# Optimization experiments

Hardware: AMD Instinct MI355X
Metric: run time of the kernel (lower is better)

## Reference

```python
import jax, jax.numpy as jnp
import numpy as np

B, S, I, H = 256, 512, 128, 256
THR = 0.001  # silence_threshold


def _glorot(k, shape):
    # xavier_uniform over the last two dims (matches nn.init.xavier_uniform_)
    fan_out, fan_in = shape[-2], shape[-1]
    lim = float(np.sqrt(6.0 / (fan_in + fan_out)))
    return jax.random.uniform(k, shape, jnp.float32, -lim, lim)


def setup_inputs() -> dict:
    key = jax.random.key(0)
    ks = jax.random.split(key, 8)
    # gate order along leading axis 0: [f, i, o, c]
    b_enc = jnp.concatenate([jnp.ones((1, H), jnp.float32), jnp.zeros((3, H), jnp.float32)], axis=0)
    return {
        "x": jax.random.normal(ks[0], (B, S, I), jnp.float32),
        # encoder: input->hidden and hidden->hidden weights (+ Linear biases + extra b_* params)
        "enc_Wx": _glorot(ks[1], (4, H, I)),
        "enc_bx": jnp.zeros((4, H), jnp.float32),
        "enc_Wh": _glorot(ks[2], (4, H, H)),
        "enc_bh": jnp.zeros((4, H), jnp.float32),
        "enc_b": b_enc,
        # decoder: its input_size == hidden_size
        "dec_Wx": _glorot(ks[3], (4, H, H)),
        "dec_bx": jnp.zeros((4, H), jnp.float32),
        "dec_Wh": _glorot(ks[4], (4, H, H)),
        "dec_bh": jnp.zeros((4, H), jnp.float32),
        "dec_b": b_enc,
        # reconstruct Linear(hidden_size -> input_size)
        "rec_W": _glorot(ks[5], (I, H)),
        "rec_b": jnp.zeros((I,), jnp.float32),
    }


def _cell(x, h, c, Wx, bx, Wh, bh, b):
    # fused gate GEMMs: g[k] = x @ Wx[k].T + bx[k] + h @ Wh[k].T + bh[k] + b[k]
    g = (jnp.einsum('bi,ghi->gbh', x, Wx) + bx[:, None, :]
         + jnp.einsum('bh,gkh->gbk', h, Wh) + bh[:, None, :]
         + b[:, None, :])  # [4, B, H]
    f_t = jax.nn.sigmoid(g[0])
    i_t = jax.nn.sigmoid(g[1])
    o_t = jax.nn.sigmoid(g[2])
    c_tilde = jnp.tanh(g[3])
    # silence mask on L2 norm over feature dim
    active = (jnp.linalg.norm(x, axis=1, keepdims=True) > THR).astype(x.dtype)
    c_next = f_t * c + i_t * c + active * (i_t * c_tilde)
    h_next = o_t * jnp.tanh(c_next)
    return h_next, c_next


def reference(x, enc_Wx, enc_bx, enc_Wh, enc_bh, enc_b,
              dec_Wx, dec_bx, dec_Wh, dec_bh, dec_b, rec_W, rec_b):
    Bsz, Slen = x.shape[0], x.shape[1]
    h0 = jnp.zeros((Bsz, H), x.dtype)
    c0 = jnp.zeros((Bsz, H), x.dtype)

    def enc_step(carry, xt):
        h, c = carry
        h, c = _cell(xt, h, c, enc_Wx, enc_bx, enc_Wh, enc_bh, enc_b)
        return (h, c), None

    (h_enc, c_enc), _ = jax.lax.scan(enc_step, (h0, c0), jnp.swapaxes(x, 0, 1))

    # in the decoder, decoder_input always equals h_prev (h fed back as input)
    def dec_step(carry, _):
        h, c = carry
        h, c = _cell(h, h, c, dec_Wx, dec_bx, dec_Wh, dec_bh, dec_b)
        out = h @ rec_W.T + rec_b  # [B, I]
        return (h, c), out

    _, outs = jax.lax.scan(dec_step, (h_enc, c_enc), None, length=Slen)
    return jnp.swapaxes(outs, 0, 1)  # [B, S, I]
```

## Files before the change

### kernel.cpp

```cpp
#include <hip/hip_runtime.h>
#include <cmath>

#define kB 256
#define kS 512
#define kI 128
#define kH 256

typedef __attribute__((ext_vector_type(8))) short short8;
typedef __attribute__((ext_vector_type(4))) float f32x4;
typedef unsigned long long u64;

#define AS_STRIDE 408

#define WS_HX_U64 (2 * 16 * 16 * 256)

__device__ __forceinline__ float sigmoidf_(float z) { return 1.0f / (1.0f + expf(-z)); }

__device__ __forceinline__ unsigned short f2b(float f) {
  unsigned u = __builtin_bit_cast(unsigned, f);
  unsigned r = (u + 0x7fffu + ((u >> 16) & 1u)) >> 16;
  return (unsigned short)r;
}
__device__ __forceinline__ float b2f(unsigned short s) {
  unsigned u = ((unsigned)s) << 16;
  return __builtin_bit_cast(float, u);
}
__device__ __forceinline__ void bsplit2(float f, unsigned short& h_, unsigned short& l_) {
  h_ = f2b(f);
  l_ = f2b(f - b2f(h_));
}
__device__ __forceinline__ void bsplit3(float f, unsigned short& h_, unsigned short& m_, unsigned short& l_) {
  h_ = f2b(f);
  float r1 = f - b2f(h_);
  m_ = f2b(r1);
  l_ = f2b(r1 - b2f(m_));
}

__device__ __forceinline__ void pollrow8(const u64* grp, int col, int rbase,
                                         unsigned seq16, u64* u) {
  unsigned miss = 0xffu;
  for (;;) {
    unsigned nm = 0;
#pragma unroll
    for (int j = 0; j < 8; ++j)
      if (miss & (1u << j))
        u[j] = __hip_atomic_load(grp + (size_t)(rbase + j) * 256 + col,
                                 __ATOMIC_RELAXED, __HIP_MEMORY_SCOPE_SYSTEM);
#pragma unroll
    for (int j = 0; j < 8; ++j)
      if ((miss & (1u << j)) && (unsigned)(u[j] >> 48) != seq16) nm |= 1u << j;
    if (!nm) return;
    miss = nm;
    __builtin_amdgcn_s_sleep(1);
  }
}

__launch_bounds__(512, 2)
__global__ void lstm_mfma(const float* __restrict__ x,
                          const float* __restrict__ enc_Wx, const float* __restrict__ enc_bx,
                          const float* __restrict__ enc_Wh, const float* __restrict__ enc_bh,
                          const float* __restrict__ enc_b,
                          const float* __restrict__ dec_Wx, const float* __restrict__ dec_bx,
                          const float* __restrict__ dec_Wh, const float* __restrict__ dec_bh,
                          const float* __restrict__ dec_b,
                          const float* __restrict__ rec_W, const float* __restrict__ rec_b,
                          float* __restrict__ out,
                          u64* __restrict__ hx) {
  __shared__ __align__(16) short As_h[16 * AS_STRIDE];
  __shared__ __align__(16) short As_m[16 * AS_STRIDE];
  __shared__ __align__(16) short As_l[16 * AS_STRIDE];
  __shared__ float g_scr[8 * 16 * 17];
  __shared__ float r_scr[8 * 16 * 17];
  __shared__ float red[16][16];
  __shared__ float maskS[16];

  const int tid = threadIdx.x;
  const int bt = blockIdx.x & 15;
  const int ht = blockIdx.x >> 4;
  const int b0 = bt << 4, hh0 = ht << 5;
  const int w  = tid >> 6;
  const int l  = tid & 63;
  const int fr = l & 15;
  const int gq = l >> 4;
  const int cb = tid >> 5;
  const int cq = tid & 31;
  const int hhc = hh0 + cq;
  const int col  = tid & 255;
  const int rbase = (tid >> 8) * 8;

  float be0 = enc_bx[0*kH+hhc] + enc_bh[0*kH+hhc] + enc_b[0*kH+hhc];
  float be1 = enc_bx[1*kH+hhc] + enc_bh[1*kH+hhc] + enc_b[1*kH+hhc];
  float be2 = enc_bx[2*kH+hhc] + enc_bh[2*kH+hhc] + enc_b[2*kH+hhc];
  float be3 = enc_bx[3*kH+hhc] + enc_bh[3*kH+hhc] + enc_b[3*kH+hhc];
  float bd0 = dec_bx[0*kH+hhc] + dec_bh[0*kH+hhc] + dec_b[0*kH+hhc];
  float bd1 = dec_bx[1*kH+hhc] + dec_bh[1*kH+hhc] + dec_b[1*kH+hhc];
  float bd2 = dec_bx[2*kH+hhc] + dec_bh[2*kH+hhc] + dec_b[2*kH+hhc];
  float bd3 = dec_bx[3*kH+hhc] + dec_bh[3*kH+hhc] + dec_b[3*kH+hhc];
  float recb = (ht < 4) ? rec_b[ht * 32 + cq] : 0.0f;
  float creg = 0.0f;

  const int g  = w & 3;
  const int hw = hh0 + ((w >> 2) << 4) + fr;
  short8 wfh[12], wfm[12], wfl[12];
#pragma unroll
  for (int kst = 0; kst < 12; ++kst) {
    int k = kst * 32 + gq * 8;
    const float* src = (k < 128)
        ? (enc_Wx + ((size_t)(g * kH) + hw) * kI + k)
        : (enc_Wh + ((size_t)(g * kH) + hw) * kH + (k - 128));
    short8 hi, mi, lo;
#pragma unroll
    for (int j = 0; j < 8; ++j) {
      unsigned short h_, m_, l_;
      bsplit3(src[j], h_, m_, l_);
      hi[j] = (short)h_; mi[j] = (short)m_; lo[j] = (short)l_;
    }
    wfh[kst] = hi; wfm[kst] = mi; wfl[kst] = lo;
  }

  for (int s = 0; s < kS; ++s) {
    const int par = s & 1;
    if (tid < 256 && (tid & 15) < 8) {
      const int xb = tid >> 4, xq = tid & 15;
      const float* xp = x + ((size_t)(b0 + xb) * kS + s) * kI + xq * 16;
      float arr[16];
      *(float4*)(arr + 0)  = *(const float4*)(xp + 0);
      *(float4*)(arr + 4)  = *(const float4*)(xp + 4);
      *(float4*)(arr + 8)  = *(const float4*)(xp + 8);
      *(float4*)(arr + 12) = *(const float4*)(xp + 12);
      float ss = 0.f;
      short8 H0, H1, M0, M1, L0, L1;
#pragma unroll
      for (int j = 0; j < 16; ++j) {
        float v = arr[j];
        ss += v * v;
        unsigned short h_, m_, l_;
        bsplit3(v, h_, m_, l_);
        if (j < 8) { H0[j] = (short)h_; M0[j] = (short)m_; L0[j] = (short)l_; }
        else       { H1[j-8] = (short)h_; M1[j-8] = (short)m_; L1[j-8] = (short)l_; }
      }
      *(short8*)(As_h + xb * AS_STRIDE + xq * 16)     = H0;
      *(short8*)(As_h + xb * AS_STRIDE + xq * 16 + 8) = H1;
      *(short8*)(As_m + xb * AS_STRIDE + xq * 16)     = M0;
      *(short8*)(As_m + xb * AS_STRIDE + xq * 16 + 8) = M1;
      *(short8*)(As_l + xb * AS_STRIDE + xq * 16)     = L0;
      *(short8*)(As_l + xb * AS_STRIDE + xq * 16 + 8) = L1;
      red[xb][xq] = ss;
    }
    {
      const u64* grp = hx + ((size_t)(par * 16 + bt) * 16) * 256;
      u64 u[8];
      pollrow8(grp, col, rbase, (unsigned)(s & 0xffff), u);
#pragma unroll
      for (int j = 0; j < 8; ++j) {
        As_h[(rbase + j) * AS_STRIDE + 128 + col] = (short)(unsigned short)(u[j] >> 32);
        As_m[(rbase + j) * AS_STRIDE + 128 + col] = (short)(unsigned short)(u[j] >> 16);
        As_l[(rbase + j) * AS_STRIDE + 128 + col] = (short)(unsigned short)(u[j]);
      }
    }
    __syncthreads();
    if (tid < 16) {
      float ss = 0.f;
#pragma unroll
      for (int j = 0; j < 8; ++j) ss += red[tid][j];
      maskS[tid] = (ss > 1e-6f) ? 1.0f : 0.0f;
    }
    f32x4 a0 = {0.f,0.f,0.f,0.f}, a1 = a0, a2 = a0, a3 = a0, a4 = a0, a5 = a0;
#pragma unroll
    for (int kst = 0; kst < 12; ++kst) {
      const short8 ah = *(const short8*)(As_h + fr * AS_STRIDE + kst * 32 + gq * 8);
      const short8 am = *(const short8*)(As_m + fr * AS_STRIDE + kst * 32 + gq * 8);
      const short8 al = *(const short8*)(As_l + fr * AS_STRIDE + kst * 32 + gq * 8);
      a0 = __builtin_amdgcn_mfma_f32_16x16x32_bf16(ah, wfh[kst], a0, 0, 0, 0);
      a1 = __builtin_amdgcn_mfma_f32_16x16x32_bf16(ah, wfm[kst], a1, 0, 0, 0);
      a2 = __builtin_amdgcn_mfma_f32_16x16x32_bf16(am, wfh[kst], a2, 0, 0, 0);
      a3 = __builtin_amdgcn_mfma_f32_16x16x32_bf16(ah, wfl[kst], a3, 0, 0, 0);
      a4 = __builtin_amdgcn_mfma_f32_16x16x32_bf16(am, wfm[kst], a4, 0, 0, 0);
      a5 = __builtin_amdgcn_mfma_f32_16x16x32_bf16(al, wfh[kst], a5, 0, 0, 0);
    }
    f32x4 d = (((a5 + a4) + a3) + (a2 + a1)) + a0;
#pragma unroll
    for (int i = 0; i < 4; ++i) g_scr[(w * 16 + gq * 4 + i) * 17 + fr] = d[i];
    __syncthreads();
    {
      const int hsub = (cq >> 4) * 4, fq = cq & 15;
      float gf = g_scr[((0 + hsub) * 16 + cb) * 17 + fq] + be0;
      float gi = g_scr[((1 + hsub) * 16 + cb) * 17 + fq] + be1;
      float go = g_scr[((2 + hsub) * 16 + cb) * 17 + fq] + be2;
      float gc = g_scr[((3 + hsub) * 16 + cb) * 17 + fq] + be3;
      float m  = maskS[cb];
      float f_ = sigmoidf_(gf), i_ = sigmoidf_(gi), o_ = sigmoidf_(go);
      float ct = tanhf(gc);
      creg = (f_ + i_) * creg + m * (i_ * ct);
      float hval = o_ * tanhf(creg);
      unsigned short hb, mb2, lb;
      bsplit3(hval, hb, mb2, lb);
      u64 pk = ((u64)(unsigned)((s + 1) & 0xffff) << 48) | ((u64)hb << 32) | ((u64)mb2 << 16) | (u64)lb;
      size_t wi = (((size_t)(((s + 1) & 1) * 16 + bt) * 16 + cb) * 256) + hhc;
      __hip_atomic_store(hx + wi, pk, __ATOMIC_RELAXED, __HIP_MEMORY_SCOPE_SYSTEM);
    }
  }

  short8 dwh[8], dwm[8], dwl[8];
#pragma unroll
  for (int kst = 0; kst < 8; ++kst) {
    int k = kst * 32 + gq * 8;
    const float* s1 = dec_Wx + ((size_t)(g * kH) + hw) * kH + k;
    const float* s2 = dec_Wh + ((size_t)(g * kH) + hw) * kH + k;
    short8 hi, mi, lo;
#pragma unroll
    for (int j = 0; j < 8; ++j) {
      unsigned short h_, m_, l_;
      bsplit3(s1[j] + s2[j], h_, m_, l_);
      hi[j] = (short)h_; mi[j] = (short)m_; lo[j] = (short)l_;
    }
    dwh[kst] = hi; dwm[kst] = mi; dwl[kst] = lo;
  }
  short8 rfh[2], rfl[2];
#pragma unroll
  for (int kk = 0; kk < 2; ++kk) {
    short8 hi = {0,0,0,0,0,0,0,0}, lo = hi;
    if (ht < 4) {
      int k = (2 * (w & 3) + kk) * 32 + gq * 8;
      const float* src = rec_W + ((size_t)(ht * 32 + ((w >> 2) << 4) + fr)) * kH + k;
#pragma unroll
      for (int j = 0; j < 8; ++j) {
        unsigned short h_, l_;
        bsplit2(src[j], h_, l_);
        hi[j] = (short)h_; lo[j] = (short)l_;
      }
    }
    rfh[kk] = hi; rfl[kk] = lo;
  }

  for (int t = 0; t < kS; ++t) {
    const int s = kS + t;
    const int par = s & 1;
    {
      const u64* grp = hx + ((size_t)(par * 16 + bt) * 16) * 256;
      u64 u[8];
      pollrow8(grp, col, rbase, (unsigned)(s & 0xffff), u);
#pragma unroll
      for (int j = 0; j < 8; ++j) {
        As_h[(rbase + j) * AS_STRIDE + col] = (short)(unsigned short)(u[j] >> 32);
        As_m[(rbase + j) * AS_STRIDE + col] = (short)(unsigned short)(u[j] >> 16);
        As_l[(rbase + j) * AS_STRIDE + col] = (short)(unsigned short)(u[j]);
      }
    }
    __syncthreads();
    if (tid < 256) {
      const int mb = tid >> 4, mq = tid & 15;
      float ss = 0.f;
#pragma unroll
      for (int g2 = 0; g2 < 2; ++g2) {
        const short8 hv = *(const short8*)(As_h + mb * AS_STRIDE + mq * 16 + g2 * 8);
        const short8 mv = *(const short8*)(As_m + mb * AS_STRIDE + mq * 16 + g2 * 8);
        const short8 lv = *(const short8*)(As_l + mb * AS_STRIDE + mq * 16 + g2 * 8);
#pragma unroll
        for (int j = 0; j < 8; ++j) {
          float v = b2f((unsigned short)hv[j]) + b2f((unsigned short)mv[j]) + b2f((unsigned short)lv[j]);
          ss += v * v;
        }
      }
      red[mb][mq] = ss;
    }
    __syncthreads();
    if (tid < 16) {
      float ss = 0.f;
#pragma unroll
      for (int j = 0; j < 16; ++j) ss += red[tid][j];
      maskS[tid] = (ss > 1e-6f) ? 1.0f : 0.0f;
    }
    f32x4 a0 = {0.f,0.f,0.f,0.f}, a1 = a0, a2 = a0, a3 = a0, a4 = a0, a5 = a0;
#pragma unroll
    for (int kst = 0; kst < 8; ++kst) {
      const short8 ah = *(const short8*)(As_h + fr * AS_STRIDE + kst * 32 + gq * 8);
      const short8 am = *(const short8*)(As_m + fr * AS_STRIDE + kst * 32 + gq * 8);
      const short8 al = *(const short8*)(As_l + fr * AS_STRIDE + kst * 32 + gq * 8);
      a0 = __builtin_amdgcn_mfma_f32_16x16x32_bf16(ah, dwh[kst], a0, 0, 0, 0);
      a1 = __builtin_amdgcn_mfma_f32_16x16x32_bf16(ah, dwm[kst], a1, 0, 0, 0);
      a2 = __builtin_amdgcn_mfma_f32_16x16x32_bf16(am, dwh[kst], a2, 0, 0, 0);
      a3 = __builtin_amdgcn_mfma_f32_16x16x32_bf16(ah, dwl[kst], a3, 0, 0, 0);
      a4 = __builtin_amdgcn_mfma_f32_16x16x32_bf16(am, dwm[kst], a4, 0, 0, 0);
      a5 = __builtin_amdgcn_mfma_f32_16x16x32_bf16(al, dwh[kst], a5, 0, 0, 0);
    }
    f32x4 d = (((a5 + a4) + a3) + (a2 + a1)) + a0;
#pragma unroll
    for (int i = 0; i < 4; ++i) g_scr[(w * 16 + gq * 4 + i) * 17 + fr] = d[i];
    if (ht < 4) {
      f32x4 r0 = {0.f,0.f,0.f,0.f}, r1 = r0, r2 = r0;
#pragma unroll
      for (int kk = 0; kk < 2; ++kk) {
        const short8 ah = *(const short8*)(As_h + fr * AS_STRIDE + (2 * (w & 3) + kk) * 32 + gq * 8);
        const short8 am = *(const short8*)(As_m + fr * AS_STRIDE + (2 * (w & 3) + kk) * 32 + gq * 8);
        r0 = __builtin_amdgcn_mfma_f32_16x16x32_bf16(ah, rfh[kk], r0, 0, 0, 0);
        r1 = __builtin_amdgcn_mfma_f32_16x16x32_bf16(ah, rfl[kk], r1, 0, 0, 0);
        r2 = __builtin_amdgcn_mfma_f32_16x16x32_bf16(am, rfh[kk], r2, 0, 0, 0);
      }
      f32x4 rd = r0 + r1 + r2;
#pragma unroll
      for (int i = 0; i < 4; ++i) r_scr[(w * 16 + gq * 4 + i) * 17 + fr] = rd[i];
    }
    __syncthreads();
    {
      const int hsub = (cq >> 4) * 4, fq = cq & 15;
      float gf = g_scr[((0 + hsub) * 16 + cb) * 17 + fq] + bd0;
      float gi = g_scr[((1 + hsub) * 16 + cb) * 17 + fq] + bd1;
      float go = g_scr[((2 + hsub) * 16 + cb) * 17 + fq] + bd2;
      float gc = g_scr[((3 + hsub) * 16 + cb) * 17 + fq] + bd3;
      float m  = maskS[cb];
      float f_ = sigmoidf_(gf), i_ = sigmoidf_(gi), o_ = sigmoidf_(go);
      float ct = tanhf(gc);
      creg = (f_ + i_) * creg + m * (i_ * ct);
      float hval = o_ * tanhf(creg);
      unsigned short hb, mb2, lb;
      bsplit3(hval, hb, mb2, lb);
      u64 pk = ((u64)(unsigned)((s + 1) & 0xffff) << 48) | ((u64)hb << 32) | ((u64)mb2 << 16) | (u64)lb;
      size_t wi = (((size_t)(((s + 1) & 1) * 16 + bt) * 16 + cb) * 256) + hhc;
      __hip_atomic_store(hx + wi, pk, __ATOMIC_RELAXED, __HIP_MEMORY_SCOPE_SYSTEM);
    }
    if (ht < 4 && t > 0) {
      const int c2 = cq >> 4, fq = cq & 15;
      float rsum = r_scr[((c2 * 4 + 0) * 16 + cb) * 17 + fq]
                 + r_scr[((c2 * 4 + 1) * 16 + cb) * 17 + fq]
                 + r_scr[((c2 * 4 + 2) * 16 + cb) * 17 + fq]
                 + r_scr[((c2 * 4 + 3) * 16 + cb) * 17 + fq] + recb;
      __builtin_nontemporal_store(rsum, &out[((size_t)(b0 + cb) * kS + (t - 1)) * kI + ht * 32 + cq]);
    }
  }

  {
    {
      const u64* grp = hx + ((size_t)(0 * 16 + bt) * 16) * 256;
      u64 u[8];
      pollrow8(grp, col, rbase, (unsigned)((2 * kS) & 0xffff), u);
#pragma unroll
      for (int j = 0; j < 8; ++j) {
        As_h[(rbase + j) * AS_STRIDE + col] = (short)(unsigned short)(u[j] >> 32);
        As_m[(rbase + j) * AS_STRIDE + col] = (short)(unsigned short)(u[j] >> 16);
      }
    }
    __syncthreads();
    if (ht < 4) {
      f32x4 r0 = {0.f,0.f,0.f,0.f}, r1 = r0, r2 = r0;
#pragma unroll
      for (int kk = 0; kk < 2; ++kk) {
        const short8 ah = *(const short8*)(As_h + fr * AS_STRIDE + (2 * (w & 3) + kk) * 32 + gq * 8);
        const short8 am = *(const short8*)(As_m + fr * AS_STRIDE + (2 * (w & 3) + kk) * 32 + gq * 8);
        r0 = __builtin_amdgcn_mfma_f32_16x16x32_bf16(ah, rfh[kk], r0, 0, 0, 0);
        r1 = __builtin_amdgcn_mfma_f32_16x16x32_bf16(ah, rfl[kk], r1, 0, 0, 0);
        r2 = __builtin_amdgcn_mfma_f32_16x16x32_bf16(am, rfh[kk], r2, 0, 0, 0);
      }
      f32x4 rd = r0 + r1 + r2;
#pragma unroll
      for (int i = 0; i < 4; ++i) r_scr[(w * 16 + gq * 4 + i) * 17 + fr] = rd[i];
    }
    __syncthreads();
    if (ht < 4) {
      const int c2 = cq >> 4, fq = cq & 15;
      float rsum = r_scr[((c2 * 4 + 0) * 16 + cb) * 17 + fq]
                 + r_scr[((c2 * 4 + 1) * 16 + cb) * 17 + fq]
                 + r_scr[((c2 * 4 + 2) * 16 + cb) * 17 + fq]
                 + r_scr[((c2 * 4 + 3) * 16 + cb) * 17 + fq] + recb;
      __builtin_nontemporal_store(rsum, &out[((size_t)(b0 + cb) * kS + (kS - 1)) * kI + ht * 32 + cq]);
    }
  }
}

extern "C" void kernel_launch(void* const* d_in, const int* in_sizes, int n_in,
                              void* d_out, int out_size, void* d_ws, size_t ws_size,
                              hipStream_t stream) {
  const float* x      = (const float*)d_in[0];
  const float* enc_Wx = (const float*)d_in[1];
  const float* enc_bx = (const float*)d_in[2];
  const float* enc_Wh = (const float*)d_in[3];
  const float* enc_bh = (const float*)d_in[4];
  const float* enc_b  = (const float*)d_in[5];
  const float* dec_Wx = (const float*)d_in[6];
  const float* dec_bx = (const float*)d_in[7];
  const float* dec_Wh = (const float*)d_in[8];
  const float* dec_bh = (const float*)d_in[9];
  const float* dec_b  = (const float*)d_in[10];
  const float* rec_W  = (const float*)d_in[11];
  const float* rec_b  = (const float*)d_in[12];
  float* out = (float*)d_out;

  u64* hx = (u64*)d_ws;

  hipMemsetAsync(d_ws, 0, (size_t)WS_HX_U64 * 8, stream);

  hipLaunchKernelGGL(lstm_mfma, dim3(128), dim3(512), 0, stream,
                     x, enc_Wx, enc_bx, enc_Wh, enc_bh, enc_b,
                     dec_Wx, dec_bx, dec_Wh, dec_bh, dec_b,
                     rec_W, rec_b, out, hx);
}
```

Measured before the change: 3.755 ms.

## Split gate GEMM along K across waves with two h-subtiles per wave

Each wave now computes two 16-column h subtiles over half of the K dimension instead of one subtile over full K, so each LDS A-fragment load feeds twice as many MFMAs. Partial gate sums from the two K halves are reduced through an enlarged LDS scratch before the cell update. The x load/bf16 split is spread over all 512 threads with float4 loads, and the reconstruct projection is split along K across all 8 waves with an 8-way sum. This adds accumulator registers and extra LDS reads in the reduction.

```diff
diff --git a/kernel.cpp b/kernel.cpp
--- a/kernel.cpp
+++ b/kernel.cpp
@@ -7,10 +7,12 @@
 #define kH 256
 
 typedef __attribute__((ext_vector_type(8))) short short8;
+typedef __attribute__((ext_vector_type(4))) short short4v;
 typedef __attribute__((ext_vector_type(4))) float f32x4;
 typedef unsigned long long u64;
 
 #define AS_STRIDE 408
+#define GSTR 18
 
 #define WS_HX_U64 (2 * 16 * 16 * 256)
 
@@ -55,23 +57,24 @@
   }
 }
 
-__launch_bounds__(512, 2)
-__global__ void lstm_mfma(const float* __restrict__ x,
-                          const float* __restrict__ enc_Wx, const float* __restrict__ enc_bx,
-                          const float* __restrict__ enc_Wh, const float* __restrict__ enc_bh,
-                          const float* __restrict__ enc_b,
-                          const float* __restrict__ dec_Wx, const float* __restrict__ dec_bx,
-                          const float* __restrict__ dec_Wh, const float* __restrict__ dec_bh,
-                          const float* __restrict__ dec_b,
-                          const float* __restrict__ rec_W, const float* __restrict__ rec_b,
-                          float* __restrict__ out,
-                          u64* __restrict__ hx) {
+__global__ void __launch_bounds__(512)
+__attribute__((amdgpu_waves_per_eu(2, 2)))
+lstm_mfma(const float* __restrict__ x,
+          const float* __restrict__ enc_Wx, const float* __restrict__ enc_bx,
+          const float* __restrict__ enc_Wh, const float* __restrict__ enc_bh,
+          const float* __restrict__ enc_b,
+          const float* __restrict__ dec_Wx, const float* __restrict__ dec_bx,
+          const float* __restrict__ dec_Wh, const float* __restrict__ dec_bh,
+          const float* __restrict__ dec_b,
+          const float* __restrict__ rec_W, const float* __restrict__ rec_b,
+          float* __restrict__ out,
+          u64* __restrict__ hx) {
   __shared__ __align__(16) short As_h[16 * AS_STRIDE];
   __shared__ __align__(16) short As_m[16 * AS_STRIDE];
   __shared__ __align__(16) short As_l[16 * AS_STRIDE];
-  __shared__ float g_scr[8 * 16 * 17];
-  __shared__ float r_scr[8 * 16 * 17];
-  __shared__ float red[16][16];
+  __shared__ float g_scr[16 * 16 * GSTR];
+  __shared__ float r_scr[16 * 16 * GSTR];
+  __shared__ float red[16][32];
   __shared__ float maskS[16];
 
   const int tid = threadIdx.x;
@@ -79,6 +82,8 @@
   const int ht = blockIdx.x >> 4;
   const int b0 = bt << 4, hh0 = ht << 5;
   const int w  = tid >> 6;
+  const int g  = w & 3;
+  const int kh = w >> 2;
   const int l  = tid & 63;
   const int fr = l & 15;
   const int gq = l >> 4;
@@ -99,12 +104,13 @@
   float recb = (ht < 4) ? rec_b[ht * 32 + cq] : 0.0f;
   float creg = 0.0f;
 
-  const int g  = w & 3;
-  const int hw = hh0 + ((w >> 2) << 4) + fr;
-  short8 wfh[12], wfm[12], wfl[12];
-#pragma unroll
-  for (int kst = 0; kst < 12; ++kst) {
-    int k = kst * 32 + gq * 8;
+  short8 wfh[2][6], wfm[2][6], wfl[2][6];
+#pragma unroll
+  for (int st = 0; st < 2; ++st)
+#pragma unroll
+  for (int kl = 0; kl < 6; ++kl) {
+    int k = (kh * 6 + kl) * 32 + gq * 8;
+    const int hw = hh0 + st * 16 + fr;
     const float* src = (k < 128)
         ? (enc_Wx + ((size_t)(g * kH) + hw) * kI + k)
         : (enc_Wh + ((size_t)(g * kH) + hw) * kH + (k - 128));
@@ -115,37 +121,30 @@
       bsplit3(src[j], h_, m_, l_);
       hi[j] = (short)h_; mi[j] = (short)m_; lo[j] = (short)l_;
     }
-    wfh[kst] = hi; wfm[kst] = mi; wfl[kst] = lo;
+    wfh[st][kl] = hi; wfm[st][kl] = mi; wfl[st][kl] = lo;
   }
 
   for (int s = 0; s < kS; ++s) {
     const int par = s & 1;
-    if (tid < 256 && (tid & 15) < 8) {
-      const int xb = tid >> 4, xq = tid & 15;
-      const float* xp = x + ((size_t)(b0 + xb) * kS + s) * kI + xq * 16;
-      float arr[16];
-      *(float4*)(arr + 0)  = *(const float4*)(xp + 0);
-      *(float4*)(arr + 4)  = *(const float4*)(xp + 4);
-      *(float4*)(arr + 8)  = *(const float4*)(xp + 8);
-      *(float4*)(arr + 12) = *(const float4*)(xp + 12);
+    {
+      const int xb = tid >> 5, xc = (tid & 31) * 4;
+      const float* xp = x + ((size_t)(b0 + xb) * kS + s) * kI + xc;
+      float4 xv = *(const float4*)xp;
+      float arr[4] = {xv.x, xv.y, xv.z, xv.w};
+      short4v hv, mv, lv;
       float ss = 0.f;
-      short8 H0, H1, M0, M1, L0, L1;
-#pragma unroll
-      for (int j = 0; j < 16; ++j) {
+#pragma unroll
+      for (int j = 0; j < 4; ++j) {
         float v = arr[j];
         ss += v * v;
         unsigned short h_, m_, l_;
         bsplit3(v, h_, m_, l_);
-        if (j < 8) { H0[j] = (short)h_; M0[j] = (short)m_; L0[j] = (short)l_; }
-        else       { H1[j-8] = (short)h_; M1[j-8] = (short)m_; L1[j-8] = (short)l_; }
-      }
-      *(short8*)(As_h + xb * AS_STRIDE + xq * 16)     = H0;
-      *(short8*)(As_h + xb * AS_STRIDE + xq * 16 + 8) = H1;
-      *(short8*)(As_m + xb * AS_STRIDE + xq * 16)     = M0;
-      *(short8*)(As_m + xb * AS_STRIDE + xq * 16 + 8) = M1;
-      *(short8*)(As_l + xb * AS_STRIDE + xq * 16)     = L0;
-      *(short8*)(As_l + xb * AS_STRIDE + xq * 16 + 8) = L1;
-      red[xb][xq] = ss;
+        hv[j] = (short)h_; mv[j] = (short)m_; lv[j] = (short)l_;
+      }
+      *(short4v*)(As_h + xb * AS_STRIDE + xc) = hv;
+      *(short4v*)(As_m + xb * AS_STRIDE + xc) = mv;
+      *(short4v*)(As_l + xb * AS_STRIDE + xc) = lv;
+      red[xb][tid & 31] = ss;
     }
     {
       const u64* grp = hx + ((size_t)(par * 16 + bt) * 16) * 256;
@@ -162,32 +161,44 @@
     if (tid < 16) {
       float ss = 0.f;
 #pragma unroll
-      for (int j = 0; j < 8; ++j) ss += red[tid][j];
+      for (int j = 0; j < 32; ++j) ss += red[tid][j];
       maskS[tid] = (ss > 1e-6f) ? 1.0f : 0.0f;
     }
-    f32x4 a0 = {0.f,0.f,0.f,0.f}, a1 = a0, a2 = a0, a3 = a0, a4 = a0, a5 = a0;
-#pragma unroll
-    for (int kst = 0; kst < 12; ++kst) {
-      const short8 ah = *(const short8*)(As_h + fr * AS_STRIDE + kst * 32 + gq * 8);
-      const short8 am = *(const short8*)(As_m + fr * AS_STRIDE + kst * 32 + gq * 8);
-      const short8 al = *(const short8*)(As_l + fr * AS_STRIDE + kst * 32 + gq * 8);
-      a0 = __builtin_amdgcn_mfma_f32_16x16x32_bf16(ah, wfh[kst], a0, 0, 0, 0);
-      a1 = __builtin_amdgcn_mfma_f32_16x16x32_bf16(ah, wfm[kst], a1, 0, 0, 0);
-      a2 = __builtin_amdgcn_mfma_f32_16x16x32_bf16(am, wfh[kst], a2, 0, 0, 0);
-      a3 = __builtin_amdgcn_mfma_f32_16x16x32_bf16(ah, wfl[kst], a3, 0, 0, 0);
-      a4 = __builtin_amdgcn_mfma_f32_16x16x32_bf16(am, wfm[kst], a4, 0, 0, 0);
-      a5 = __builtin_amdgcn_mfma_f32_16x16x32_bf16(al, wfh[kst], a5, 0, 0, 0);
-    }
-    f32x4 d = (((a5 + a4) + a3) + (a2 + a1)) + a0;
-#pragma unroll
-    for (int i = 0; i < 4; ++i) g_scr[(w * 16 + gq * 4 + i) * 17 + fr] = d[i];
-    __syncthreads();
-    {
-      const int hsub = (cq >> 4) * 4, fq = cq & 15;
-      float gf = g_scr[((0 + hsub) * 16 + cb) * 17 + fq] + be0;
-      float gi = g_scr[((1 + hsub) * 16 + cb) * 17 + fq] + be1;
-      float go = g_scr[((2 + hsub) * 16 + cb) * 17 + fq] + be2;
-      float gc = g_scr[((3 + hsub) * 16 + cb) * 17 + fq] + be3;
+    f32x4 acc[2][6];
+#pragma unroll
+    for (int st = 0; st < 2; ++st)
+#pragma unroll
+    for (int i = 0; i < 6; ++i) acc[st][i] = (f32x4){0.f, 0.f, 0.f, 0.f};
+#pragma unroll
+    for (int kl = 0; kl < 6; ++kl) {
+      const int ko = (kh * 6 + kl) * 32 + gq * 8;
+      const short8 ah = *(const short8*)(As_h + fr * AS_STRIDE + ko);
+      const short8 am = *(const short8*)(As_m + fr * AS_STRIDE + ko);
+      const short8 al = *(const short8*)(As_l + fr * AS_STRIDE + ko);
+#pragma unroll
+      for (int st = 0; st < 2; ++st) {
+        acc[st][0] = __builtin_amdgcn_mfma_f32_16x16x32_bf16(ah, wfh[st][kl], acc[st][0], 0, 0, 0);
+        acc[st][1] = __builtin_amdgcn_mfma_f32_16x16x32_bf16(ah, wfm[st][kl], acc[st][1], 0, 0, 0);
+        acc[st][2] = __builtin_amdgcn_mfma_f32_16x16x32_bf16(am, wfh[st][kl], acc[st][2], 0, 0, 0);
+        acc[st][3] = __builtin_amdgcn_mfma_f32_16x16x32_bf16(ah, wfl[st][kl], acc[st][3], 0, 0, 0);
+        acc[st][4] = __builtin_amdgcn_mfma_f32_16x16x32_bf16(am, wfm[st][kl], acc[st][4], 0, 0, 0);
+        acc[st][5] = __builtin_amdgcn_mfma_f32_16x16x32_bf16(al, wfh[st][kl], acc[st][5], 0, 0, 0);
+      }
+    }
+#pragma unroll
+    for (int st = 0; st < 2; ++st) {
+      f32x4 d = (((acc[st][5] + acc[st][4]) + acc[st][3]) + (acc[st][2] + acc[st][1])) + acc[st][0];
+      const int ti = (kh * 4 + g) * 2 + st;
+#pragma unroll
+      for (int i = 0; i < 4; ++i) g_scr[(ti * 16 + gq * 4 + i) * GSTR + fr] = d[i];
+    }
+    __syncthreads();
+    {
+      const int st = cq >> 4, fq = cq & 15;
+      float gf = g_scr[(((0*4+0)*2+st)*16+cb)*GSTR+fq] + g_scr[(((1*4+0)*2+st)*16+cb)*GSTR+fq] + be0;
+      float gi = g_scr[(((0*4+1)*2+st)*16+cb)*GSTR+fq] + g_scr[(((1*4+1)*2+st)*16+cb)*GSTR+fq] + be1;
+      float go = g_scr[(((0*4+2)*2+st)*16+cb)*GSTR+fq] + g_scr[(((1*4+2)*2+st)*16+cb)*GSTR+fq] + be2;
+      float gc = g_scr[(((0*4+3)*2+st)*16+cb)*GSTR+fq] + g_scr[(((1*4+3)*2+st)*16+cb)*GSTR+fq] + be3;
       float m  = maskS[cb];
       float f_ = sigmoidf_(gf), i_ = sigmoidf_(gi), o_ = sigmoidf_(go);
       float ct = tanhf(gc);
@@ -201,10 +212,13 @@
     }
   }
 
-  short8 dwh[8], dwm[8], dwl[8];
-#pragma unroll
-  for (int kst = 0; kst < 8; ++kst) {
-    int k = kst * 32 + gq * 8;
+  short8 dwh[2][4], dwm[2][4], dwl[2][4];
+#pragma unroll
+  for (int st = 0; st < 2; ++st)
+#pragma unroll
+  for (int kl = 0; kl < 4; ++kl) {
+    int k = (kh * 4 + kl) * 32 + gq * 8;
+    const int hw = hh0 + st * 16 + fr;
     const float* s1 = dec_Wx + ((size_t)(g * kH) + hw) * kH + k;
     const float* s2 = dec_Wh + ((size_t)(g * kH) + hw) * kH + k;
     short8 hi, mi, lo;
@@ -214,15 +228,15 @@
       bsplit3(s1[j] + s2[j], h_, m_, l_);
       hi[j] = (short)h_; mi[j] = (short)m_; lo[j] = (short)l_;
     }
-    dwh[kst] = hi; dwm[kst] = mi; dwl[kst] = lo;
+    dwh[st][kl] = hi; dwm[st][kl] = mi; dwl[st][kl] = lo;
   }
   short8 rfh[2], rfl[2];
 #pragma unroll
-  for (int kk = 0; kk < 2; ++kk) {
+  for (int st = 0; st < 2; ++st) {
     short8 hi = {0,0,0,0,0,0,0,0}, lo = hi;
     if (ht < 4) {
-      int k = (2 * (w & 3) + kk) * 32 + gq * 8;
-      const float* src = rec_W + ((size_t)(ht * 32 + ((w >> 2) << 4) + fr)) * kH + k;
+      int k = w * 32 + gq * 8;
+      const float* src = rec_W + ((size_t)(ht * 32 + st * 16 + fr)) * kH + k;
 #pragma unroll
       for (int j = 0; j < 8; ++j) {
         unsigned short h_, l_;
@@ -230,7 +244,7 @@
         hi[j] = (short)h_; lo[j] = (short)l_;
       }
     }
-    rfh[kk] = hi; rfl[kk] = lo;
+    rfh[st] = hi; rfl[st] = lo;
   }
 
   for (int t = 0; t < kS; ++t) {
@@ -271,43 +285,56 @@
       for (int j = 0; j < 16; ++j) ss += red[tid][j];
       maskS[tid] = (ss > 1e-6f) ? 1.0f : 0.0f;
     }
-    f32x4 a0 = {0.f,0.f,0.f,0.f}, a1 = a0, a2 = a0, a3 = a0, a4 = a0, a5 = a0;
-#pragma unroll
-    for (int kst = 0; kst < 8; ++kst) {
-      const short8 ah = *(const short8*)(As_h + fr * AS_STRIDE + kst * 32 + gq * 8);
-      const short8 am = *(const short8*)(As_m + fr * AS_STRIDE + kst * 32 + gq * 8);
-      const short8 al = *(const short8*)(As_l + fr * AS_STRIDE + kst * 32 + gq * 8);
-      a0 = __builtin_amdgcn_mfma_f32_16x16x32_bf16(ah, dwh[kst], a0, 0, 0, 0);
-      a1 = __builtin_amdgcn_mfma_f32_16x16x32_bf16(ah, dwm[kst], a1, 0, 0, 0);
-      a2 = __builtin_amdgcn_mfma_f32_16x16x32_bf16(am, dwh[kst], a2, 0, 0, 0);
-      a3 = __builtin_amdgcn_mfma_f32_16x16x32_bf16(ah, dwl[kst], a3, 0, 0, 0);
-      a4 = __builtin_amdgcn_mfma_f32_16x16x32_bf16(am, dwm[kst], a4, 0, 0, 0);
-      a5 = __builtin_amdgcn_mfma_f32_16x16x32_bf16(al, dwh[kst], a5, 0, 0, 0);
-    }
-    f32x4 d = (((a5 + a4) + a3) + (a2 + a1)) + a0;
-#pragma unroll
-    for (int i = 0; i < 4; ++i) g_scr[(w * 16 + gq * 4 + i) * 17 + fr] = d[i];
+    f32x4 acc[2][6];
+#pragma unroll
+    for (int st = 0; st < 2; ++st)
+#pragma unroll
+    for (int i = 0; i < 6; ++i) acc[st][i] = (f32x4){0.f, 0.f, 0.f, 0.f};
+#pragma unroll
+    for (int kl = 0; kl < 4; ++kl) {
+      const int ko = (kh * 4 + kl) * 32 + gq * 8;
+      const short8 ah = *(const short8*)(As_h + fr * AS_STRIDE + ko);
+      const short8 am = *(const short8*)(As_m + fr * AS_STRIDE + ko);
+      const short8 al = *(const short8*)(As_l + fr * AS_STRIDE + ko);
+#pragma unroll
+      for (int st = 0; st < 2; ++st) {
+        acc[st][0] = __builtin_amdgcn_mfma_f32_16x16x32_bf16(ah, dwh[st][kl], acc[st][0], 0, 0, 0);
+        acc[st][1] = __builtin_amdgcn_mfma_f32_16x16x32_bf16(ah, dwm[st][kl], acc[st][1], 0, 0, 0);
+        acc[st][2] = __builtin_amdgcn_mfma_f32_16x16x32_bf16(am, dwh[st][kl], acc[st][2], 0, 0, 0);
+        acc[st][3] = __builtin_amdgcn_mfma_f32_16x16x32_bf16(ah, dwl[st][kl], acc[st][3], 0, 0, 0);
+        acc[st][4] = __builtin_amdgcn_mfma_f32_16x16x32_bf16(am, dwm[st][kl], acc[st][4], 0, 0, 0);
+        acc[st][5] = __builtin_amdgcn_mfma_f32_16x16x32_bf16(al, dwh[st][kl], acc[st][5], 0, 0, 0);
+      }
+    }
+#pragma unroll
+    for (int st = 0; st < 2; ++st) {
+      f32x4 d = (((acc[st][5] + acc[st][4]) + acc[st][3]) + (acc[st][2] + acc[st][1])) + acc[st][0];
+      const int ti = (kh * 4 + g) * 2 + st;
+#pragma unroll
+      for (int i = 0; i < 4; ++i) g_scr[(ti * 16 + gq * 4 + i) * GSTR + fr] = d[i];
+    }
     if (ht < 4) {
-      f32x4 r0 = {0.f,0.f,0.f,0.f}, r1 = r0, r2 = r0;
-#pragma unroll
-      for (int kk = 0; kk < 2; ++kk) {
-        const short8 ah = *(const short8*)(As_h + fr * AS_STRIDE + (2 * (w & 3) + kk) * 32 + gq * 8);
-        const short8 am = *(const short8*)(As_m + fr * AS_STRIDE + (2 * (w & 3) + kk) * 32 + gq * 8);
-        r0 = __builtin_amdgcn_mfma_f32_16x16x32_bf16(ah, rfh[kk], r0, 0, 0, 0);
-        r1 = __builtin_amdgcn_mfma_f32_16x16x32_bf16(ah, rfl[kk], r1, 0, 0, 0);
-        r2 = __builtin_amdgcn_mfma_f32_16x16x32_bf16(am, rfh[kk], r2, 0, 0, 0);
-      }
-      f32x4 rd = r0 + r1 + r2;
-#pragma unroll
-      for (int i = 0; i < 4; ++i) r_scr[(w * 16 + gq * 4 + i) * 17 + fr] = rd[i];
-    }
-    __syncthreads();
-    {
-      const int hsub = (cq >> 4) * 4, fq = cq & 15;
-      float gf = g_scr[((0 + hsub) * 16 + cb) * 17 + fq] + bd0;
-      float gi = g_scr[((1 + hsub) * 16 + cb) * 17 + fq] + bd1;
-      float go = g_scr[((2 + hsub) * 16 + cb) * 17 + fq] + bd2;
-      float gc = g_scr[((3 + hsub) * 16 + cb) * 17 + fq] + bd3;
+      const int ko = w * 32 + gq * 8;
+      const short8 ah = *(const short8*)(As_h + fr * AS_STRIDE + ko);
+      const short8 am = *(const short8*)(As_m + fr * AS_STRIDE + ko);
+#pragma unroll
+      for (int st = 0; st < 2; ++st) {
+        f32x4 r0 = {0.f,0.f,0.f,0.f}, r1 = r0, r2 = r0;
+        r0 = __builtin_amdgcn_mfma_f32_16x16x32_bf16(ah, rfh[st], r0, 0, 0, 0);
+        r1 = __builtin_amdgcn_mfma_f32_16x16x32_bf16(ah, rfl[st], r1, 0, 0, 0);
+        r2 = __builtin_amdgcn_mfma_f32_16x16x32_bf16(am, rfh[st], r2, 0, 0, 0);
+        f32x4 rd = r0 + r1 + r2;
+#pragma unroll
+        for (int i = 0; i < 4; ++i) r_scr[((w * 2 + st) * 16 + gq * 4 + i) * GSTR + fr] = rd[i];
+      }
+    }
+    __syncthreads();
+    {
+      const int st = cq >> 4, fq = cq & 15;
+      float gf = g_scr[(((0*4+0)*2+st)*16+cb)*GSTR+fq] + g_scr[(((1*4+0)*2+st)*16+cb)*GSTR+fq] + bd0;
+      float gi = g_scr[(((0*4+1)*2+st)*16+cb)*GSTR+fq] + g_scr[(((1*4+1)*2+st)*16+cb)*GSTR+fq] + bd1;
+      float go = g_scr[(((0*4+2)*2+st)*16+cb)*GSTR+fq] + g_scr[(((1*4+2)*2+st)*16+cb)*GSTR+fq] + bd2;
+      float gc = g_scr[(((0*4+3)*2+st)*16+cb)*GSTR+fq] + g_scr[(((1*4+3)*2+st)*16+cb)*GSTR+fq] + bd3;
       float m  = maskS[cb];
       float f_ = sigmoidf_(gf), i_ = sigmoidf_(gi), o_ = sigmoidf_(go);
       float ct = tanhf(gc);
@@ -320,11 +347,11 @@
       __hip_atomic_store(hx + wi, pk, __ATOMIC_RELAXED, __HIP_MEMORY_SCOPE_SYSTEM);
     }
     if (ht < 4 && t > 0) {
-      const int c2 = cq >> 4, fq = cq & 15;
-      float rsum = r_scr[((c2 * 4 + 0) * 16 + cb) * 17 + fq]
-                 + r_scr[((c2 * 4 + 1) * 16 + cb) * 17 + fq]
-                 + r_scr[((c2 * 4 + 2) * 16 + cb) * 17 + fq]
-                 + r_scr[((c2 * 4 + 3) * 16 + cb) * 17 + fq] + recb;
+      const int st = cq >> 4, fq = cq & 15;
+      float rsum = recb;
+#pragma unroll
+      for (int ww = 0; ww < 8; ++ww)
+        rsum += r_scr[((ww * 2 + st) * 16 + cb) * GSTR + fq];
       __builtin_nontemporal_store(rsum, &out[((size_t)(b0 + cb) * kS + (t - 1)) * kI + ht * 32 + cq]);
     }
   }
@@ -342,26 +369,27 @@
     }
     __syncthreads();
     if (ht < 4) {
-      f32x4 r0 = {0.f,0.f,0.f,0.f}, r1 = r0, r2 = r0;
-#pragma unroll
-      for (int kk = 0; kk < 2; ++kk) {
-        const short8 ah = *(const short8*)(As_h + fr * AS_STRIDE + (2 * (w & 3) + kk) * 32 + gq * 8);
-        const short8 am = *(const short8*)(As_m + fr * AS_STRIDE + (2 * (w & 3) + kk) * 32 + gq * 8);
-        r0 = __builtin_amdgcn_mfma_f32_16x16x32_bf16(ah, rfh[kk], r0, 0, 0, 0);
-        r1 = __builtin_amdgcn_mfma_f32_16x16x32_bf16(ah, rfl[kk], r1, 0, 0, 0);
-        r2 = __builtin_amdgcn_mfma_f32_16x16x32_bf16(am, rfh[kk], r2, 0, 0, 0);
-      }
-      f32x4 rd = r0 + r1 + r2;
-#pragma unroll
-      for (int i = 0; i < 4; ++i) r_scr[(w * 16 + gq * 4 + i) * 17 + fr] = rd[i];
+      const int ko = w * 32 + gq * 8;
+      const short8 ah = *(const short8*)(As_h + fr * AS_STRIDE + ko);
+      const short8 am = *(const short8*)(As_m + fr * AS_STRIDE + ko);
+#pragma unroll
+      for (int st = 0; st < 2; ++st) {
+        f32x4 r0 = {0.f,0.f,0.f,0.f}, r1 = r0, r2 = r0;
+        r0 = __builtin_amdgcn_mfma_f32_16x16x32_bf16(ah, rfh[st], r0, 0, 0, 0);
+        r1 = __builtin_amdgcn_mfma_f32_16x16x32_bf16(ah, rfl[st], r1, 0, 0, 0);
+        r2 = __builtin_amdgcn_mfma_f32_16x16x32_bf16(am, rfh[st], r2, 0, 0, 0);
+        f32x4 rd = r0 + r1 + r2;
+#pragma unroll
+        for (int i = 0; i < 4; ++i) r_scr[((w * 2 + st) * 16 + gq * 4 + i) * GSTR + fr] = rd[i];
+      }
     }
     __syncthreads();
     if (ht < 4) {
-      const int c2 = cq >> 4, fq = cq & 15;
-      float rsum = r_scr[((c2 * 4 + 0) * 16 + cb) * 17 + fq]
-                 + r_scr[((c2 * 4 + 1) * 16 + cb) * 17 + fq]
-                 + r_scr[((c2 * 4 + 2) * 16 + cb) * 17 + fq]
-                 + r_scr[((c2 * 4 + 3) * 16 + cb) * 17 + fq] + recb;
+      const int st = cq >> 4, fq = cq & 15;
+      float rsum = recb;
+#pragma unroll
+      for (int ww = 0; ww < 8; ++ww)
+        rsum += r_scr[((ww * 2 + st) * 16 + cb) * GSTR + fq];
       __builtin_nontemporal_store(rsum, &out[((size_t)(b0 + cb) * kS + (kS - 1)) * kI + ht * 32 + cq]);
     }
   }
```

New measurement: 4.746 ms. 26.4% more time.

## Overlap x-part MFMAs with hidden-state polling and spread x load over all threads

Applied to the files above, without the earlier changes.

In the encoder loop, all 512 threads now load and split x with one float4 each, not 128 threads with 16 each. A barrier then lets the x-input MFMAs (k-steps 0-3) run before the cross-block poll for the previous hidden state, so that part of the GEMM overlaps the wait. The decoder norm reduction is likewise spread over all threads with one short8 per array. This adds an extra barrier per encoder step and a wider reduction buffer.

```diff
diff --git a/kernel.cpp b/kernel.cpp
--- a/kernel.cpp
+++ b/kernel.cpp
@@ -7,6 +7,7 @@
 #define kH 256
 
 typedef __attribute__((ext_vector_type(8))) short short8;
+typedef __attribute__((ext_vector_type(4))) short short4v;
 typedef __attribute__((ext_vector_type(4))) float f32x4;
 typedef unsigned long long u64;
 
@@ -71,7 +72,7 @@
   __shared__ __align__(16) short As_l[16 * AS_STRIDE];
   __shared__ float g_scr[8 * 16 * 17];
   __shared__ float r_scr[8 * 16 * 17];
-  __shared__ float red[16][16];
+  __shared__ float red[16][32];
   __shared__ float maskS[16];
 
   const int tid = threadIdx.x;
@@ -120,32 +121,39 @@
 
   for (int s = 0; s < kS; ++s) {
     const int par = s & 1;
-    if (tid < 256 && (tid & 15) < 8) {
-      const int xb = tid >> 4, xq = tid & 15;
-      const float* xp = x + ((size_t)(b0 + xb) * kS + s) * kI + xq * 16;
-      float arr[16];
-      *(float4*)(arr + 0)  = *(const float4*)(xp + 0);
-      *(float4*)(arr + 4)  = *(const float4*)(xp + 4);
-      *(float4*)(arr + 8)  = *(const float4*)(xp + 8);
-      *(float4*)(arr + 12) = *(const float4*)(xp + 12);
+    {
+      const int xb = tid >> 5, xc = (tid & 31) * 4;
+      const float* xp = x + ((size_t)(b0 + xb) * kS + s) * kI + xc;
+      float4 xv = *(const float4*)xp;
+      float arr[4] = {xv.x, xv.y, xv.z, xv.w};
+      short4v hv, mv, lv;
       float ss = 0.f;
-      short8 H0, H1, M0, M1, L0, L1;
-#pragma unroll
-      for (int j = 0; j < 16; ++j) {
+#pragma unroll
+      for (int j = 0; j < 4; ++j) {
         float v = arr[j];
         ss += v * v;
         unsigned short h_, m_, l_;
         bsplit3(v, h_, m_, l_);
-        if (j < 8) { H0[j] = (short)h_; M0[j] = (short)m_; L0[j] = (short)l_; }
-        else       { H1[j-8] = (short)h_; M1[j-8] = (short)m_; L1[j-8] = (short)l_; }
-      }
-      *(short8*)(As_h + xb * AS_STRIDE + xq * 16)     = H0;
-      *(short8*)(As_h + xb * AS_STRIDE + xq * 16 + 8) = H1;
-      *(short8*)(As_m + xb * AS_STRIDE + xq * 16)     = M0;
-      *(short8*)(As_m + xb * AS_STRIDE + xq * 16 + 8) = M1;
-      *(short8*)(As_l + xb * AS_STRIDE + xq * 16)     = L0;
-      *(short8*)(As_l + xb * AS_STRIDE + xq * 16 + 8) = L1;
-      red[xb][xq] = ss;
+        hv[j] = (short)h_; mv[j] = (short)m_; lv[j] = (short)l_;
+      }
+      *(short4v*)(As_h + xb * AS_STRIDE + xc) = hv;
+      *(short4v*)(As_m + xb * AS_STRIDE + xc) = mv;
+      *(short4v*)(As_l + xb * AS_STRIDE + xc) = lv;
+      red[xb][tid & 31] = ss;
+    }
+    __syncthreads();
+    f32x4 a0 = {0.f,0.f,0.f,0.f}, a1 = a0, a2 = a0, a3 = a0, a4 = a0, a5 = a0;
+#pragma unroll
+    for (int kst = 0; kst < 4; ++kst) {
+      const short8 ah = *(const short8*)(As_h + fr * AS_STRIDE + kst * 32 + gq * 8);
+      const short8 am = *(const short8*)(As_m + fr * AS_STRIDE + kst * 32 + gq * 8);
+      const short8 al = *(const short8*)(As_l + fr * AS_STRIDE + kst * 32 + gq * 8);
+      a0 = __builtin_amdgcn_mfma_f32_16x16x32_bf16(ah, wfh[kst], a0, 0, 0, 0);
+      a1 = __builtin_amdgcn_mfma_f32_16x16x32_bf16(ah, wfm[kst], a1, 0, 0, 0);
+      a2 = __builtin_amdgcn_mfma_f32_16x16x32_bf16(am, wfh[kst], a2, 0, 0, 0);
+      a3 = __builtin_amdgcn_mfma_f32_16x16x32_bf16(ah, wfl[kst], a3, 0, 0, 0);
+      a4 = __builtin_amdgcn_mfma_f32_16x16x32_bf16(am, wfm[kst], a4, 0, 0, 0);
+      a5 = __builtin_amdgcn_mfma_f32_16x16x32_bf16(al, wfh[kst], a5, 0, 0, 0);
     }
     {
       const u64* grp = hx + ((size_t)(par * 16 + bt) * 16) * 256;
@@ -162,12 +170,11 @@
     if (tid < 16) {
       float ss = 0.f;
 #pragma unroll
-      for (int j = 0; j < 8; ++j) ss += red[tid][j];
+      for (int j = 0; j < 32; ++j) ss += red[tid][j];
       maskS[tid] = (ss > 1e-6f) ? 1.0f : 0.0f;
     }
-    f32x4 a0 = {0.f,0.f,0.f,0.f}, a1 = a0, a2 = a0, a3 = a0, a4 = a0, a5 = a0;
-#pragma unroll
-    for (int kst = 0; kst < 12; ++kst) {
+#pragma unroll
+    for (int kst = 4; kst < 12; ++kst) {
       const short8 ah = *(const short8*)(As_h + fr * AS_STRIDE + kst * 32 + gq * 8);
       const short8 am = *(const short8*)(As_m + fr * AS_STRIDE + kst * 32 + gq * 8);
       const short8 al = *(const short8*)(As_l + fr * AS_STRIDE + kst * 32 + gq * 8);
@@ -248,27 +255,24 @@
       }
     }
     __syncthreads();
-    if (tid < 256) {
-      const int mb = tid >> 4, mq = tid & 15;
+    {
+      const int mb = tid >> 5, c0 = (tid & 31) * 8;
+      const short8 hv = *(const short8*)(As_h + mb * AS_STRIDE + c0);
+      const short8 mv = *(const short8*)(As_m + mb * AS_STRIDE + c0);
+      const short8 lv = *(const short8*)(As_l + mb * AS_STRIDE + c0);
       float ss = 0.f;
 #pragma unroll
-      for (int g2 = 0; g2 < 2; ++g2) {
-        const short8 hv = *(const short8*)(As_h + mb * AS_STRIDE + mq * 16 + g2 * 8);
-        const short8 mv = *(const short8*)(As_m + mb * AS_STRIDE + mq * 16 + g2 * 8);
-        const short8 lv = *(const short8*)(As_l + mb * AS_STRIDE + mq * 16 + g2 * 8);
-#pragma unroll
-        for (int j = 0; j < 8; ++j) {
-          float v = b2f((unsigned short)hv[j]) + b2f((unsigned short)mv[j]) + b2f((unsigned short)lv[j]);
-          ss += v * v;
-        }
-      }
-      red[mb][mq] = ss;
+      for (int j = 0; j < 8; ++j) {
+        float v = b2f((unsigned short)hv[j]) + b2f((unsigned short)mv[j]) + b2f((unsigned short)lv[j]);
+        ss += v * v;
+      }
+      red[mb][tid & 31] = ss;
     }
     __syncthreads();
     if (tid < 16) {
       float ss = 0.f;
 #pragma unroll
-      for (int j = 0; j < 16; ++j) ss += red[tid][j];
+      for (int j = 0; j < 32; ++j) ss += red[tid][j];
       maskS[tid] = (ss > 1e-6f) ? 1.0f : 0.0f;
     }
     f32x4 a0 = {0.f,0.f,0.f,0.f}, a1 = a0, a2 = a0, a3 = a0, a4 = a0, a5 = a0;
```

Result: slower. 4.221 ms (+12.4%).
